# Optimization experiments

Hardware: AMD Instinct MI355X
Metric: run time of the kernel (lower is better)

Reference implementation:

```python
import jax, jax.numpy as jnp
import numpy as np


def setup_inputs() -> dict:
    key = jax.random.key(0)
    k1, k2, k3, k4 = jax.random.split(key, 4)
    n, d, h, w = 16, 512, 64, 64
    m, kcodes = 4, 256
    dm = d // m  # 128
    latent = jax.random.normal(k1, (n, d, h, w), dtype=jnp.float32)
    codebook = jax.random.normal(k2, (m, kcodes, dm), dtype=jnp.float32)
    wq = jax.random.normal(k3, (m, dm, dm), dtype=jnp.float32) / np.sqrt(dm)
    wk = jax.random.normal(k4, (m, dm, dm), dtype=jnp.float32) / np.sqrt(dm)
    return {"latent": latent, "codebook": codebook, "wq": wq, "wk": wk}


def reference(latent, codebook, wq, wk):
    # latent: [n, d, h, w]; codebook: [m, k, dm]; wq/wk: [m, dm, dm]
    n, d, h, w = latent.shape
    m, kcodes, dm = codebook.shape
    # NCHW -> NHWC -> [n, h, w, m, dm]
    q = jnp.transpose(latent, (0, 2, 3, 1)).reshape(n, h, w, m, dm)
    # per-group query projection: q @ wq^T (einsum 'nhwmd,mcd->nhwmc')
    q = jnp.einsum('nhwmd,mcd->nhwmc', q, wq)
    # per-group key projection of codebook: 'mkd,mcd->mkc'
    keys = jnp.einsum('mkd,mcd->mkc', codebook, wk)
    # dot-product scores over code dim, then argmax -> code indices
    scores = jnp.einsum('nhwmd,mkd->nhwmk', q, keys)
    code = jnp.argmax(scores, axis=-1).astype(jnp.uint8)
    return code
```

## Files before the change

kernel.cpp:

```cpp
#include <hip/hip_runtime.h>


#define MM   4
#define KC   256
#define DM   128
#define HW   4096
#define WW_  64
#define EPS  0.045f
#define WL_CAP 65536
#define RSH  136

typedef _Float16 f16x8 __attribute__((ext_vector_type(8)));
typedef _Float16 f16x4 __attribute__((ext_vector_type(4)));
typedef _Float16 f16x2 __attribute__((ext_vector_type(2)));
typedef float    f32x4 __attribute__((ext_vector_type(4)));

__global__ __launch_bounds__(128) void a_kernel(const float* __restrict__ wk,
                                                const float* __restrict__ wq,
                                                double* __restrict__ A) {
    int me = blockIdx.x;
    int d  = threadIdx.x;
    int m  = me >> 7;
    int e  = me & 127;
    const float* wkm = wk + (size_t)m * DM * DM + e;
    const float* wqm = wq + (size_t)m * DM * DM + d;
    double s0 = 0.0, s1 = 0.0, s2 = 0.0, s3 = 0.0;
#pragma unroll 8
    for (int c = 0; c < DM; c += 4) {
        s0 = fma((double)wkm[(size_t)(c+0) * DM], (double)wqm[(size_t)(c+0) * DM], s0);
        s1 = fma((double)wkm[(size_t)(c+1) * DM], (double)wqm[(size_t)(c+1) * DM], s1);
        s2 = fma((double)wkm[(size_t)(c+2) * DM], (double)wqm[(size_t)(c+2) * DM], s2);
        s3 = fma((double)wkm[(size_t)(c+3) * DM], (double)wqm[(size_t)(c+3) * DM], s3);
    }
    A[(size_t)me * DM + d] = (s0 + s1) + (s2 + s3);
}

__global__ __launch_bounds__(128) void keff_kernel(const float* __restrict__ cb,
                                                   const double* __restrict__ A,
                                                   double* __restrict__ keffdT,
                                                   _Float16* __restrict__ keff16) {
    int mk = blockIdx.x;
    int d  = threadIdx.x;
    int m  = mk >> 8;
    int k  = mk & 255;
    const float*  cbr = cb + (size_t)mk * DM;
    const double* Am  = A + (size_t)m * DM * DM + d;
    double s0 = 0.0, s1 = 0.0, s2 = 0.0, s3 = 0.0;
#pragma unroll 8
    for (int e = 0; e < DM; e += 4) {
        s0 = fma((double)cbr[e+0], Am[(size_t)(e+0) * DM], s0);
        s1 = fma((double)cbr[e+1], Am[(size_t)(e+1) * DM], s1);
        s2 = fma((double)cbr[e+2], Am[(size_t)(e+2) * DM], s2);
        s3 = fma((double)cbr[e+3], Am[(size_t)(e+3) * DM], s3);
    }
    double s = (s0 + s1) + (s2 + s3);
    keffdT[((size_t)m * DM + d) * KC + k] = s;
    keff16[(size_t)mk * DM + d] = (_Float16)s;
}

__global__ __launch_bounds__(256, 3) void argmax_mfma(const float* __restrict__ latent,
                                                      const _Float16* __restrict__ keff16,
                                                      int* __restrict__ out,
                                                      int* __restrict__ wl_cnt,
                                                      int* __restrict__ wl) {
    __shared__ _Float16 lq[2][64 * RSH];
    __shared__ float pbv[64][4];
    __shared__ float psv[64][4];
    __shared__ int   pbi[64][4];

    int blk  = blockIdx.x;
    int n    = blk >> 6;
    int m    = (blk >> 4) & 3;
    int hg   = blk & 15;
    int tid  = threadIdx.x;
    int wave = tid >> 6;
    int lane = tid & 63;
    int col  = lane & 15;
    int quad = lane >> 4;
    int w4   = (tid & 15) * 4;
    int db   = (tid >> 4) * 8;

    f16x8 Af[4][4];
    {
        const _Float16* kbase = keff16 + ((size_t)m * KC + wave * 64) * DM;
#pragma unroll
        for (int t = 0; t < 4; ++t)
#pragma unroll
            for (int s = 0; s < 4; ++s)
                Af[t][s] = *(const f16x8*)(kbase + (size_t)(t * 16 + col) * DM + s * 32 + quad * 8);
    }

    const float* lp0 = latent + ((size_t)(n * 512 + m * DM)) * HW + (size_t)(hg * 4) * WW_;

    {
        f32x4 pf[8];
#pragma unroll
        for (int pp = 0; pp < 8; ++pp)
            pf[pp] = *(const f32x4*)(lp0 + (size_t)(db + pp) * HW + w4);
#pragma unroll
        for (int j = 0; j < 4; ++j) {
            f16x8 v;
#pragma unroll
            for (int pp = 0; pp < 8; ++pp) v[pp] = (_Float16)pf[pp][j];
            *(f16x8*)&lq[0][(size_t)(w4 + j) * RSH + db] = v;
        }
    }
    __syncthreads();

    for (int r = 0; r < 4; ++r) {
        int cur = r & 1;

        f32x4 pf[8];
        if (r < 3) {
            const float* lp = lp0 + (size_t)(r + 1) * WW_;
#pragma unroll
            for (int pp = 0; pp < 8; ++pp)
                pf[pp] = *(const f32x4*)(lp + (size_t)(db + pp) * HW + w4);
        }

#pragma unroll
        for (int p = 0; p < 4; ++p) {
            f16x8 Bf[4];
#pragma unroll
            for (int s = 0; s < 4; ++s)
                Bf[s] = *(const f16x8*)&lq[cur][(size_t)(p * 16 + col) * RSH + s * 32 + quad * 8];
            f32x4 acc[4];
#pragma unroll
            for (int t = 0; t < 4; ++t) {
                f32x4 c = (f32x4){0.f, 0.f, 0.f, 0.f};
                c = __builtin_amdgcn_mfma_f32_16x16x32_f16(Af[t][0], Bf[0], c, 0, 0, 0);
                c = __builtin_amdgcn_mfma_f32_16x16x32_f16(Af[t][1], Bf[1], c, 0, 0, 0);
                c = __builtin_amdgcn_mfma_f32_16x16x32_f16(Af[t][2], Bf[2], c, 0, 0, 0);
                c = __builtin_amdgcn_mfma_f32_16x16x32_f16(Af[t][3], Bf[3], c, 0, 0, 0);
                acc[t] = c;
            }
            float bv = acc[0][0];
            int   bi = wave * 64 + quad * 4;
            float sv = -3.0e38f;
#pragma unroll
            for (int t = 0; t < 4; ++t)
#pragma unroll
                for (int g = 0; g < 4; ++g) {
                    if (t == 0 && g == 0) continue;
                    float v   = acc[t][g];
                    int   idx = wave * 64 + t * 16 + quad * 4 + g;
                    if (v > bv)      { sv = bv; bv = v; bi = idx; }
                    else if (v > sv) sv = v;
                }
#pragma unroll
            for (int off = 16; off < 64; off <<= 1) {
                float ov = __shfl_xor(bv, off);
                int   oi = __shfl_xor(bi, off);
                float os = __shfl_xor(sv, off);
                bool  take  = (ov > bv) || (ov == bv && oi < bi);
                float loser = take ? bv : ov;
                sv = fmaxf(fmaxf(sv, os), loser);
                if (take) { bv = ov; bi = oi; }
            }
            if (quad == 0) {
                int P = p * 16 + col;
                pbv[P][wave] = bv; psv[P][wave] = sv; pbi[P][wave] = bi;
            }
        }
        __syncthreads();

        if (tid < 64) {
            int   P  = tid;
            float bv = pbv[P][0]; float sv = psv[P][0]; int bi = pbi[P][0];
#pragma unroll
            for (int wv = 1; wv < 4; ++wv) {
                float ov = pbv[P][wv]; float os = psv[P][wv]; int oi = pbi[P][wv];
                bool  take  = (ov > bv) || (ov == bv && oi < bi);
                float loser = take ? bv : ov;
                sv = fmaxf(fmaxf(sv, os), loser);
                if (take) { bv = ov; bi = oi; }
            }
            int h   = hg * 4 + r;
            int pix = (((n * 64 + h) * 64) + P) * MM + m;
            out[pix] = bi;
            if (bv - sv < EPS) {
                int slot = atomicAdd(wl_cnt, 1);
                if (slot < WL_CAP) wl[slot] = pix;
            }
        }

        if (r < 3) {
#pragma unroll
            for (int j = 0; j < 4; ++j) {
                f16x8 v;
#pragma unroll
                for (int pp = 0; pp < 8; ++pp) v[pp] = (_Float16)pf[pp][j];
                *(f16x8*)&lq[cur ^ 1][(size_t)(w4 + j) * RSH + db] = v;
            }
        }
        __syncthreads();
    }
}

__global__ __launch_bounds__(256) void rescue_kernel(const float* __restrict__ latent,
                                                     const double* __restrict__ keffdT,
                                                     const int* __restrict__ wl_cnt,
                                                     const int* __restrict__ wl,
                                                     int* __restrict__ out) {
    __shared__ double sq[DM];
    __shared__ double svals[256];
    __shared__ int    sidx[256];
    int cnt = *wl_cnt;
    if (cnt > WL_CAP) cnt = WL_CAP;
    int t = threadIdx.x;
    for (int i = blockIdx.x; i < cnt; i += gridDim.x) {
        int pix = wl[i];
        int m   = pix & 3;
        int rem = pix >> 2;
        int w   = rem & 63;
        int bh  = rem >> 6;
        int n   = bh >> 6;
        int h   = bh & 63;
        const float* lp = latent + ((size_t)(n * 512 + m * DM)) * HW + h * WW_ + w;
        if (t < DM) sq[t] = (double)lp[(size_t)t * HW];
        __syncthreads();
        const double* kr = keffdT + (size_t)m * DM * KC + t;
        double s0 = 0.0, s1 = 0.0, s2 = 0.0, s3 = 0.0;
#pragma unroll 8
        for (int d = 0; d < DM; d += 4) {
            s0 = fma(sq[d+0], kr[(size_t)(d+0) * KC], s0);
            s1 = fma(sq[d+1], kr[(size_t)(d+1) * KC], s1);
            s2 = fma(sq[d+2], kr[(size_t)(d+2) * KC], s2);
            s3 = fma(sq[d+3], kr[(size_t)(d+3) * KC], s3);
        }
        svals[t] = (s0 + s1) + (s2 + s3);
        sidx[t]  = t;
        __syncthreads();
        for (int stp = 128; stp > 0; stp >>= 1) {
            if (t < stp) {
                double vo = svals[t + stp], vm = svals[t];
                int io = sidx[t + stp], im = sidx[t];
                if (vo > vm || (vo == vm && io < im)) { svals[t] = vo; sidx[t] = io; }
            }
            __syncthreads();
        }
        if (t == 0) out[pix] = sidx[0];
        __syncthreads();
    }
}

extern "C" void kernel_launch(void* const* d_in, const int* in_sizes, int n_in,
                              void* d_out, int out_size, void* d_ws, size_t ws_size,
                              hipStream_t stream) {
    const float* latent = (const float*)d_in[0];
    const float* cb     = (const float*)d_in[1];
    const float* wq     = (const float*)d_in[2];
    const float* wk     = (const float*)d_in[3];
    int* out = (int*)d_out;

    char* ws = (char*)d_ws;
    double*   A      = (double*)ws;     ws += (size_t)MM * DM * DM * sizeof(double);
    double*   keffdT = (double*)ws;     ws += (size_t)MM * DM * KC * sizeof(double);
    _Float16* keff16 = (_Float16*)ws;   ws += (size_t)MM * KC * DM * sizeof(_Float16);
    int*      wl_cnt = (int*)ws;        ws += 256;
    int*      wl     = (int*)ws;

    hipMemsetAsync(wl_cnt, 0, sizeof(int), stream);
    a_kernel<<<MM * DM, 128, 0, stream>>>(wk, wq, A);
    keff_kernel<<<MM * KC, 128, 0, stream>>>(cb, A, keffdT, keff16);
    argmax_mfma<<<1024, 256, 0, stream>>>(latent, keff16, out, wl_cnt, wl);
    rescue_kernel<<<1024, 256, 0, stream>>>(latent, keffdT, wl_cnt, wl, out);
}
```

Baseline: 283.1 us.

## Split rescue worklist per group and batch sixteen pixels per rescue block

The near-tie worklist is split into four per-group lists, each with its own counter padded to a separate cache line, which reduces contention on a single global atomic. The rescue kernel now handles 16 pixels per block, with 16 threads per pixel each scoring 16 codes in fp64. Partial argmaxes are combined with xor shuffles instead of a shared-memory tree reduction with a barrier per step. This amortises the keff loads and barriers over more pixels, but each group's list is now capped at 16384 entries.

```diff
diff --git a/kernel.cpp b/kernel.cpp
--- a/kernel.cpp
+++ b/kernel.cpp
@@ -7,7 +7,8 @@
 #define HW   4096
 #define WW_  64
 #define EPS  0.045f
-#define WL_CAP 65536
+#define WLC  16384
+#define PIXB 16
 #define RSH  136
 
 typedef _Float16 f16x8 __attribute__((ext_vector_type(8)));
@@ -179,8 +180,8 @@
             int pix = (((n * 64 + h) * 64) + P) * MM + m;
             out[pix] = bi;
             if (bv - sv < EPS) {
-                int slot = atomicAdd(wl_cnt, 1);
-                if (slot < WL_CAP) wl[slot] = pix;
+                int slot = atomicAdd(wl_cnt + m * 16, 1);
+                if (slot < WLC) wl[m * WLC + slot] = pix;
             }
         }
 
@@ -202,44 +203,59 @@
                                                      const int* __restrict__ wl_cnt,
                                                      const int* __restrict__ wl,
                                                      int* __restrict__ out) {
-    __shared__ double sq[DM];
-    __shared__ double svals[256];
-    __shared__ int    sidx[256];
-    int cnt = *wl_cnt;
-    if (cnt > WL_CAP) cnt = WL_CAP;
-    int t = threadIdx.x;
-    for (int i = blockIdx.x; i < cnt; i += gridDim.x) {
-        int pix = wl[i];
-        int m   = pix & 3;
-        int rem = pix >> 2;
-        int w   = rem & 63;
-        int bh  = rem >> 6;
-        int n   = bh >> 6;
-        int h   = bh & 63;
+    __shared__ double sq[PIXB][DM];
+    __shared__ int    spix[PIXB];
+    int b   = blockIdx.x;
+    int m   = b & 3;
+    int t   = threadIdx.x;
+    int pi  = t >> 4;
+    int kg  = t & 15;
+    int cnt = wl_cnt[m * 16];
+    if (cnt > WLC) cnt = WLC;
+    const int*    wlm = wl + m * WLC;
+    const double* krm = keffdT + (size_t)m * DM * KC;
+
+    for (int c0 = (b >> 2) * PIXB; c0 < cnt; c0 += 256 * PIXB) {
+        int idx  = c0 + pi;
+        int vld  = idx < cnt;
+        int pix  = wlm[vld ? idx : c0];
+        int rem  = pix >> 2;
+        int w    = rem & 63;
+        int bh   = rem >> 6;
+        int n    = bh >> 6;
+        int h    = bh & 63;
         const float* lp = latent + ((size_t)(n * 512 + m * DM)) * HW + h * WW_ + w;
-        if (t < DM) sq[t] = (double)lp[(size_t)t * HW];
-        __syncthreads();
-        const double* kr = keffdT + (size_t)m * DM * KC + t;
-        double s0 = 0.0, s1 = 0.0, s2 = 0.0, s3 = 0.0;
-#pragma unroll 8
-        for (int d = 0; d < DM; d += 4) {
-            s0 = fma(sq[d+0], kr[(size_t)(d+0) * KC], s0);
-            s1 = fma(sq[d+1], kr[(size_t)(d+1) * KC], s1);
-            s2 = fma(sq[d+2], kr[(size_t)(d+2) * KC], s2);
-            s3 = fma(sq[d+3], kr[(size_t)(d+3) * KC], s3);
-        }
-        svals[t] = (s0 + s1) + (s2 + s3);
-        sidx[t]  = t;
-        __syncthreads();
-        for (int stp = 128; stp > 0; stp >>= 1) {
-            if (t < stp) {
-                double vo = svals[t + stp], vm = svals[t];
-                int io = sidx[t + stp], im = sidx[t];
-                if (vo > vm || (vo == vm && io < im)) { svals[t] = vo; sidx[t] = io; }
-            }
-            __syncthreads();
-        }
-        if (t == 0) out[pix] = sidx[0];
+#pragma unroll
+        for (int dd = 0; dd < 8; ++dd) {
+            int d = kg * 8 + dd;
+            sq[pi][d] = (double)lp[(size_t)d * HW];
+        }
+        if (kg == 0) spix[pi] = vld ? pix : -1;
+        __syncthreads();
+
+        double s[16];
+#pragma unroll
+        for (int j = 0; j < 16; ++j) s[j] = 0.0;
+        const double* kb = krm + kg;
+        for (int d = 0; d < DM; ++d) {
+            double qd = sq[pi][d];
+            const double* kd = kb + (size_t)d * KC;
+#pragma unroll
+            for (int j = 0; j < 16; ++j)
+                s[j] = fma(qd, kd[(size_t)j * 16], s[j]);
+        }
+        double bv = s[0]; int bi = kg;
+#pragma unroll
+        for (int j = 1; j < 16; ++j)
+            if (s[j] > bv) { bv = s[j]; bi = j * 16 + kg; }
+#pragma unroll
+        for (int off = 1; off < 16; off <<= 1) {
+            double ov = __shfl_xor(bv, off);
+            int    oi = __shfl_xor(bi, off);
+            if (ov > bv || (ov == bv && oi < bi)) { bv = ov; bi = oi; }
+        }
+        int opix = spix[pi];
+        if (kg == 0 && opix >= 0) out[opix] = bi;
         __syncthreads();
     }
 }
@@ -260,7 +276,7 @@
     int*      wl_cnt = (int*)ws;        ws += 256;
     int*      wl     = (int*)ws;
 
-    hipMemsetAsync(wl_cnt, 0, sizeof(int), stream);
+    hipMemsetAsync(wl_cnt, 0, 256, stream);
     a_kernel<<<MM * DM, 128, 0, stream>>>(wk, wq, A);
     keff_kernel<<<MM * KC, 128, 0, stream>>>(cb, A, keffdT, keff16);
     argmax_mfma<<<1024, 256, 0, stream>>>(latent, keff16, out, wl_cnt, wl);
```

After: 302.8 us. 1.07x slower.
